# Optimization experiments

Measured on AMD Instinct MI355X. Metric: run time of the kernel, lower is better.

Reference implementation:

```python
import jax, jax.numpy as jnp
import numpy as np

# EntNet entity-memory update (Henaff et al. 2017), per selected entity i:
#   g_i      = sigmoid(s . h_i + s . w_i)                       (gate)
#   h~_i     = relu(h_i @ U^T + w_i @ V^T + s @ W^T)            (candidate)
#   h_i      = l2_normalize(h_i + g_i * h~_i)
# The original TF code loops over `indices` in Python; since each index touches a
# distinct entity slot, the updates are independent and we vectorize with a single
# gather over the entity axis and a scatter (.at[].set) back.

def setup_inputs() -> dict:
    key = jax.random.key(0)
    ks = jax.random.split(key, 6)
    B, N, D, K = 32, 1024, 1024, 512
    return {
        "encoded_sents": jax.random.normal(ks[0], (B, D), jnp.float32),
        "hiddens": jax.random.normal(ks[1], (B, N, D), jnp.float32),
        "keys": jax.random.normal(ks[2], (B, N, D), jnp.float32),
        "U": jax.random.normal(ks[3], (D, D), jnp.float32),
        "V": jax.random.normal(ks[4], (D, D), jnp.float32),
        "W": jax.random.normal(ks[5], (D, D), jnp.float32),
        "indices": jnp.arange(K, dtype=jnp.int64),
    }

def reference(encoded_sents, hiddens, keys, U, V, W, indices):
    EPS = 1e-12
    h = hiddens[:, indices, :]                     # [B,K,D] gather selected entities
    w = keys[:, indices, :]                        # [B,K,D]
    s = encoded_sents                              # [B,D]
    # gate: sigmoid(s.h_i + s.w_i) -> [B,K]
    g = jax.nn.sigmoid(jnp.einsum('bd,bkd->bk', s, h + w))
    # candidate: relu(h U^T + w V^T + s W^T) -> [B,K,D]
    h_tilde = jax.nn.relu(
        jnp.einsum('bkd,ed->bke', h, U)
        + jnp.einsum('bkd,ed->bke', w, V)
        + (s @ W.T)[:, None, :]
    )
    h_new = h + g[..., None] * h_tilde
    # tf.math.l2_normalize: x * rsqrt(max(sum(x^2), eps))
    h_new = h_new * jax.lax.rsqrt(jnp.maximum(jnp.sum(h_new * h_new, axis=-1, keepdims=True), EPS))
    # scatter updated entities back
    return hiddens.at[:, indices, :].set(h_new)
```

## Files before the change

kernel.cpp:

```cpp
#include <hip/hip_runtime.h>

constexpr int Bb = 32;
constexpr int Nn = 1024;
constexpr int Dd = 1024;
constexpr int Kk = 512;
constexpr int Mm = Bb * Kk;
constexpr int KD = 2 * Dd;

using bf16x8 = __bf16 __attribute__((ext_vector_type(8)));
using f32x4  = float __attribute__((ext_vector_type(4)));

constexpr size_t WS_BBF = 0;
constexpr size_t WS_G   = (size_t)4 * 1024 * 1024;
constexpr size_t WS_SW  = WS_G + 64 * 1024;
constexpr size_t WS_RN  = WS_SW + 128 * 1024;

__global__ void prep_b_kernel(const float* __restrict__ U,
                              const float* __restrict__ V,
                              __bf16* __restrict__ Bbf) {
  int t = blockIdx.x * 256 + threadIdx.x;
  int e = t >> 8;
  int c = (t & 255) << 3;
  const float* src = (c < Dd) ? (U + (size_t)e * Dd + c)
                              : (V + (size_t)e * Dd + (c - Dd));
  f32x4 f0 = *(const f32x4*)src;
  f32x4 f1 = *(const f32x4*)(src + 4);
  bf16x8 v;
  v[0] = (__bf16)f0[0]; v[1] = (__bf16)f0[1]; v[2] = (__bf16)f0[2]; v[3] = (__bf16)f0[3];
  v[4] = (__bf16)f1[0]; v[5] = (__bf16)f1[1]; v[6] = (__bf16)f1[2]; v[7] = (__bf16)f1[3];
  *(bf16x8*)(Bbf + (size_t)e * KD + c) = v;
}

__global__ void sw_kernel(const float* __restrict__ s,
                          const float* __restrict__ W,
                          float* __restrict__ sW) {
  int e = blockIdx.x * 4 + (threadIdx.x >> 6);
  int lane = threadIdx.x & 63;
  const float* wp = W + (size_t)e * Dd;
  float wr[16];
#pragma unroll
  for (int c = 0; c < 4; c++) {
    f32x4 wv = *(const f32x4*)(wp + c * 256 + lane * 4);
    wr[c*4+0] = wv[0]; wr[c*4+1] = wv[1]; wr[c*4+2] = wv[2]; wr[c*4+3] = wv[3];
  }
  for (int b = 0; b < Bb; b++) {
    const float* sp = s + (size_t)b * Dd;
    float acc = 0.f;
#pragma unroll
    for (int c = 0; c < 4; c++) {
      f32x4 sv = *(const f32x4*)(sp + c * 256 + lane * 4);
      acc += sv[0]*wr[c*4+0] + sv[1]*wr[c*4+1] + sv[2]*wr[c*4+2] + sv[3]*wr[c*4+3];
    }
#pragma unroll
    for (int off = 32; off; off >>= 1) acc += __shfl_xor(acc, off);
    if (lane == 0) sW[b * Nn + e] = acc;
  }
}

__global__ void g_kernel(const float* __restrict__ s,
                         const float* __restrict__ hiddens,
                         const float* __restrict__ keys,
                         const int* __restrict__ idx,
                         float* __restrict__ g) {
  int wid = blockIdx.x * 4 + (threadIdx.x >> 6);
  int lane = threadIdx.x & 63;
  int b = wid >> 9;
  int k = wid & (Kk - 1);
  int row = idx[k];
  const float* hp = hiddens + ((size_t)(b * Nn + row)) * Dd;
  const float* wp = keys    + ((size_t)(b * Nn + row)) * Dd;
  const float* sp = s + (size_t)b * Dd;
  float acc = 0.f;
#pragma unroll
  for (int c = 0; c < 4; c++) {
    int d = c * 256 + lane * 4;
    f32x4 hv = *(const f32x4*)(hp + d);
    f32x4 wv = *(const f32x4*)(wp + d);
    f32x4 sv = *(const f32x4*)(sp + d);
    acc += sv[0]*(hv[0]+wv[0]) + sv[1]*(hv[1]+wv[1])
         + sv[2]*(hv[2]+wv[2]) + sv[3]*(hv[3]+wv[3]);
  }
#pragma unroll
  for (int off = 32; off; off >>= 1) acc += __shfl_xor(acc, off);
  if (lane == 0) g[wid] = 1.f / (1.f + expf(-acc));
}

__global__ __launch_bounds__(256)
void gemm_kernel(const float* __restrict__ hiddens,
                 const float* __restrict__ keys,
                 const int* __restrict__ idx,
                 const __bf16* __restrict__ Bbf,
                 const float* __restrict__ sW,
                 const float* __restrict__ g,
                 float* __restrict__ rownorm,
                 float* __restrict__ out) {
  __shared__ __bf16 a_lds[128 * 64];
  __shared__ __bf16 b_lds[128 * 64];

  int bid = blockIdx.x;
  int mt = bid >> 3;
  int nt = bid & 7;
  int m0 = mt * 128, e0 = nt * 128;
  int tid = threadIdx.x, lane = tid & 63, wave = tid >> 6;

  size_t roff[4]; int prow[4], pcol[4];
#pragma unroll
  for (int i = 0; i < 4; i++) {
    int p = tid + i * 256;
    int row = p >> 3;
    pcol[i] = (p & 7) * 8;
    prow[i] = row;
    int m = m0 + row;
    int b = m >> 9;
    int r = idx[m & (Kk - 1)];
    roff[i] = ((size_t)(b * Nn + r)) * Dd;
  }
  int bofs[4], brow[4], bcolb[4];
#pragma unroll
  for (int i = 0; i < 4; i++) {
    int o = (wave * 4 + i) * 1024 + lane * 16;
    bofs[i] = o;
    brow[i] = o >> 7;
    bcolb[i] = o & 127;
  }

  f32x4 acc[4][4] = {};
  int wm = (wave >> 1) * 64, we = (wave & 1) * 64;
  int lr = lane & 15, lg = lane >> 4;
  const char* BbfB = (const char*)Bbf;

  for (int t = 0; t < KD / 64; ++t) {
    int kd0 = t * 64;
    const float* Asrc = (kd0 < Dd) ? hiddens : keys;
    int d0 = kd0 & (Dd - 1);

#pragma unroll
    for (int i = 0; i < 4; i++) {
      const void* gp = BbfB + ((size_t)(e0 + brow[i]) * KD + kd0) * 2 + bcolb[i];
      __builtin_amdgcn_global_load_lds(
          (const __attribute__((address_space(1))) void*)gp,
          (__attribute__((address_space(3))) void*)((char*)b_lds + bofs[i]),
          16, 0, 0);
    }
#pragma unroll
    for (int i = 0; i < 4; i++) {
      const float* src = Asrc + roff[i] + d0 + pcol[i];
      f32x4 f0 = *(const f32x4*)src;
      f32x4 f1 = *(const f32x4*)(src + 4);
      bf16x8 v;
      v[0]=(__bf16)f0[0]; v[1]=(__bf16)f0[1]; v[2]=(__bf16)f0[2]; v[3]=(__bf16)f0[3];
      v[4]=(__bf16)f1[0]; v[5]=(__bf16)f1[1]; v[6]=(__bf16)f1[2]; v[7]=(__bf16)f1[3];
      *(bf16x8*)&a_lds[prow[i] * 64 + pcol[i]] = v;
    }
    __syncthreads();

#pragma unroll
    for (int kh = 0; kh < 2; ++kh) {
      bf16x8 af[4], bfr[4];
#pragma unroll
      for (int i = 0; i < 4; i++)
        af[i] = *(const bf16x8*)&a_lds[(wm + i * 16 + lr) * 64 + kh * 32 + lg * 8];
#pragma unroll
      for (int j = 0; j < 4; j++)
        bfr[j] = *(const bf16x8*)&b_lds[(we + j * 16 + lr) * 64 + kh * 32 + lg * 8];
#pragma unroll
      for (int i = 0; i < 4; i++)
#pragma unroll
        for (int j = 0; j < 4; j++)
          acc[i][j] = __builtin_amdgcn_mfma_f32_16x16x32_bf16(af[i], bfr[j], acc[i][j], 0, 0, 0);
    }
    __syncthreads();
  }

#pragma unroll
  for (int i = 0; i < 4; i++) {
#pragma unroll
    for (int r = 0; r < 4; r++) {
      int m = m0 + wm + i * 16 + lg * 4 + r;
      int b = m >> 9;
      int rowidx = idx[m & (Kk - 1)];
      size_t base = ((size_t)(b * Nn + rowidx)) * Dd;
      float gg = g[m];
      float part = 0.f;
#pragma unroll
      for (int j = 0; j < 4; j++) {
        int e = e0 + we + j * 16 + lr;
        float ht = acc[i][j][r] + sW[b * Nn + e];
        ht = fmaxf(ht, 0.f);
        float v = hiddens[base + e] + gg * ht;
        out[base + e] = v;
        part += v * v;
      }
      part += __shfl_xor(part, 1);
      part += __shfl_xor(part, 2);
      part += __shfl_xor(part, 4);
      part += __shfl_xor(part, 8);
      if (lr == 0) atomicAdd(&rownorm[m], part);
    }
  }
}

__global__ void norm_kernel(const int* __restrict__ idx,
                            const float* __restrict__ rownorm,
                            float* __restrict__ out) {
  int m = blockIdx.x;
  int b = m >> 9;
  int rowidx = idx[m & (Kk - 1)];
  float nr = fmaxf(rownorm[m], 1e-12f);
  float y = rsqrtf(nr);
  y = y * (1.5f - 0.5f * nr * y * y);
  f32x4* p = (f32x4*)(out + ((size_t)(b * Nn + rowidx)) * Dd);
  f32x4 v = p[threadIdx.x];
  v[0] *= y; v[1] *= y; v[2] *= y; v[3] *= y;
  p[threadIdx.x] = v;
}

extern "C" void kernel_launch(void* const* d_in, const int* in_sizes, int n_in,
                              void* d_out, int out_size, void* d_ws, size_t ws_size,
                              hipStream_t stream) {
  const float* s       = (const float*)d_in[0];
  const float* hiddens = (const float*)d_in[1];
  const float* keys    = (const float*)d_in[2];
  const float* U       = (const float*)d_in[3];
  const float* V       = (const float*)d_in[4];
  const float* W       = (const float*)d_in[5];
  const int*   idx     = (const int*)d_in[6];
  float* out = (float*)d_out;

  char* ws = (char*)d_ws;
  __bf16* Bbf    = (__bf16*)(ws + WS_BBF);
  float*  g      = (float*)(ws + WS_G);
  float*  sW     = (float*)(ws + WS_SW);
  float*  rnorm  = (float*)(ws + WS_RN);

  hipMemcpyAsync(out, hiddens, (size_t)out_size * sizeof(float),
                 hipMemcpyDeviceToDevice, stream);
  hipMemsetAsync(rnorm, 0, Mm * sizeof(float), stream);
  prep_b_kernel<<<1024, 256, 0, stream>>>(U, V, Bbf);
  sw_kernel<<<Nn / 4, 256, 0, stream>>>(s, W, sW);
  g_kernel<<<Mm / 4, 256, 0, stream>>>(s, hiddens, keys, idx, g);
  gemm_kernel<<<(Mm / 128) * (Nn / 128), 256, 0, stream>>>(
      hiddens, keys, idx, Bbf, sW, g, rnorm, out);
  norm_kernel<<<Mm, 256, 0, stream>>>(idx, rnorm, out);
}
```

Before: 540.4 us.

## Pre-pack gathered A to bf16, async-load both GEMM operands, copy only unselected rows

The gate kernel now also converts the gathered h and w rows to a contiguous bf16 A matrix. The GEMM then streams both operands straight into LDS with global_load_lds instead of converting fp32 in registers. The full hiddens memcpy is replaced by a masked copy kernel that skips rows the GEMM overwrites. The tile order is changed so consecutive blocks share the same B column tile. The cost is a 64MB bf16 workspace write and read, plus extra mask and copy kernel launches.

New measurement: 519.4 us. -3.9%, faster.

```diff
diff --git a/kernel.cpp b/kernel.cpp
--- a/kernel.cpp
+++ b/kernel.cpp
@@ -10,10 +10,29 @@
 using bf16x8 = __bf16 __attribute__((ext_vector_type(8)));
 using f32x4  = float __attribute__((ext_vector_type(4)));
 
-constexpr size_t WS_BBF = 0;
-constexpr size_t WS_G   = (size_t)4 * 1024 * 1024;
-constexpr size_t WS_SW  = WS_G + 64 * 1024;
-constexpr size_t WS_RN  = WS_SW + 128 * 1024;
+constexpr size_t WS_ABF  = 0;
+constexpr size_t WS_BBF  = (size_t)Mm * KD * 2;
+constexpr size_t WS_G    = WS_BBF + (size_t)Nn * KD * 2;
+constexpr size_t WS_SW   = WS_G + Mm * sizeof(float);
+constexpr size_t WS_RN   = WS_SW + Bb * Nn * sizeof(float);
+constexpr size_t WS_MASK = WS_RN + Mm * sizeof(float);
+
+__global__ void mask_kernel(const int* __restrict__ idx, int* __restrict__ mask) {
+  int t = threadIdx.x;
+  mask[t] = 0;
+  __syncthreads();
+  if (t < Kk) mask[idx[t]] = 1;
+}
+
+__global__ void copy_kernel(const float* __restrict__ hiddens,
+                            const int* __restrict__ mask,
+                            float* __restrict__ out) {
+  int bid = blockIdx.x;
+  int n = bid & (Nn - 1);
+  if (mask[n]) return;
+  size_t base = (size_t)bid * Dd + threadIdx.x * 4;
+  *(f32x4*)(out + base) = *(const f32x4*)(hiddens + base);
+}
 
 __global__ void prep_b_kernel(const float* __restrict__ U,
                               const float* __restrict__ V,
@@ -57,100 +76,96 @@
   }
 }
 
-__global__ void g_kernel(const float* __restrict__ s,
-                         const float* __restrict__ hiddens,
-                         const float* __restrict__ keys,
-                         const int* __restrict__ idx,
-                         float* __restrict__ g) {
-  int wid = blockIdx.x * 4 + (threadIdx.x >> 6);
+__global__ void pack_g_kernel(const float* __restrict__ s,
+                              const float* __restrict__ hiddens,
+                              const float* __restrict__ keys,
+                              const int* __restrict__ idx,
+                              __bf16* __restrict__ Abf,
+                              float* __restrict__ g) {
+  int m = blockIdx.x * 4 + (threadIdx.x >> 6);
   int lane = threadIdx.x & 63;
-  int b = wid >> 9;
-  int k = wid & (Kk - 1);
+  int b = m >> 9;
+  int k = m & (Kk - 1);
   int row = idx[k];
   const float* hp = hiddens + ((size_t)(b * Nn + row)) * Dd;
   const float* wp = keys    + ((size_t)(b * Nn + row)) * Dd;
   const float* sp = s + (size_t)b * Dd;
+  __bf16* ap = Abf + (size_t)m * KD;
+
   float acc = 0.f;
 #pragma unroll
-  for (int c = 0; c < 4; c++) {
-    int d = c * 256 + lane * 4;
-    f32x4 hv = *(const f32x4*)(hp + d);
-    f32x4 wv = *(const f32x4*)(wp + d);
-    f32x4 sv = *(const f32x4*)(sp + d);
-    acc += sv[0]*(hv[0]+wv[0]) + sv[1]*(hv[1]+wv[1])
-         + sv[2]*(hv[2]+wv[2]) + sv[3]*(hv[3]+wv[3]);
+  for (int c = 0; c < 2; c++) {
+    int d = c * 512 + lane * 8;
+    f32x4 h0 = *(const f32x4*)(hp + d);
+    f32x4 h1 = *(const f32x4*)(hp + d + 4);
+    f32x4 w0 = *(const f32x4*)(wp + d);
+    f32x4 w1 = *(const f32x4*)(wp + d + 4);
+    f32x4 s0 = *(const f32x4*)(sp + d);
+    f32x4 s1 = *(const f32x4*)(sp + d + 4);
+    acc += s0[0]*(h0[0]+w0[0]) + s0[1]*(h0[1]+w0[1])
+         + s0[2]*(h0[2]+w0[2]) + s0[3]*(h0[3]+w0[3])
+         + s1[0]*(h1[0]+w1[0]) + s1[1]*(h1[1]+w1[1])
+         + s1[2]*(h1[2]+w1[2]) + s1[3]*(h1[3]+w1[3]);
+    bf16x8 hv, wv;
+    hv[0]=(__bf16)h0[0]; hv[1]=(__bf16)h0[1]; hv[2]=(__bf16)h0[2]; hv[3]=(__bf16)h0[3];
+    hv[4]=(__bf16)h1[0]; hv[5]=(__bf16)h1[1]; hv[6]=(__bf16)h1[2]; hv[7]=(__bf16)h1[3];
+    wv[0]=(__bf16)w0[0]; wv[1]=(__bf16)w0[1]; wv[2]=(__bf16)w0[2]; wv[3]=(__bf16)w0[3];
+    wv[4]=(__bf16)w1[0]; wv[5]=(__bf16)w1[1]; wv[6]=(__bf16)w1[2]; wv[7]=(__bf16)w1[3];
+    *(bf16x8*)(ap + d) = hv;
+    *(bf16x8*)(ap + Dd + d) = wv;
   }
 #pragma unroll
   for (int off = 32; off; off >>= 1) acc += __shfl_xor(acc, off);
-  if (lane == 0) g[wid] = 1.f / (1.f + expf(-acc));
+  if (lane == 0) g[m] = 1.f / (1.f + expf(-acc));
 }
 
 __global__ __launch_bounds__(256)
-void gemm_kernel(const float* __restrict__ hiddens,
-                 const float* __restrict__ keys,
+void gemm_kernel(const __bf16* __restrict__ Abf,
+                 const __bf16* __restrict__ Bbf,
                  const int* __restrict__ idx,
-                 const __bf16* __restrict__ Bbf,
                  const float* __restrict__ sW,
                  const float* __restrict__ g,
+                 const float* __restrict__ hiddens,
                  float* __restrict__ rownorm,
                  float* __restrict__ out) {
   __shared__ __bf16 a_lds[128 * 64];
   __shared__ __bf16 b_lds[128 * 64];
 
   int bid = blockIdx.x;
-  int mt = bid >> 3;
-  int nt = bid & 7;
+  int mt = bid & 127;
+  int nt = bid >> 7;
   int m0 = mt * 128, e0 = nt * 128;
   int tid = threadIdx.x, lane = tid & 63, wave = tid >> 6;
 
-  size_t roff[4]; int prow[4], pcol[4];
-#pragma unroll
-  for (int i = 0; i < 4; i++) {
-    int p = tid + i * 256;
-    int row = p >> 3;
-    pcol[i] = (p & 7) * 8;
-    prow[i] = row;
-    int m = m0 + row;
-    int b = m >> 9;
-    int r = idx[m & (Kk - 1)];
-    roff[i] = ((size_t)(b * Nn + r)) * Dd;
-  }
-  int bofs[4], brow[4], bcolb[4];
+  int lofs[4]; size_t aoff[4], boff[4];
 #pragma unroll
   for (int i = 0; i < 4; i++) {
     int o = (wave * 4 + i) * 1024 + lane * 16;
-    bofs[i] = o;
-    brow[i] = o >> 7;
-    bcolb[i] = o & 127;
+    lofs[i] = o;
+    int row = o >> 7;
+    int colb = o & 127;
+    aoff[i] = ((size_t)(m0 + row) * KD) * 2 + colb;
+    boff[i] = ((size_t)(e0 + row) * KD) * 2 + colb;
   }
 
   f32x4 acc[4][4] = {};
   int wm = (wave >> 1) * 64, we = (wave & 1) * 64;
   int lr = lane & 15, lg = lane >> 4;
-  const char* BbfB = (const char*)Bbf;
+  const char* Ab = (const char*)Abf;
+  const char* Bbp = (const char*)Bbf;
 
   for (int t = 0; t < KD / 64; ++t) {
-    int kd0 = t * 64;
-    const float* Asrc = (kd0 < Dd) ? hiddens : keys;
-    int d0 = kd0 & (Dd - 1);
-
+    size_t kb = (size_t)t * 128;
 #pragma unroll
     for (int i = 0; i < 4; i++) {
-      const void* gp = BbfB + ((size_t)(e0 + brow[i]) * KD + kd0) * 2 + bcolb[i];
       __builtin_amdgcn_global_load_lds(
-          (const __attribute__((address_space(1))) void*)gp,
-          (__attribute__((address_space(3))) void*)((char*)b_lds + bofs[i]),
+          (const __attribute__((address_space(1))) void*)(Ab + aoff[i] + kb),
+          (__attribute__((address_space(3))) void*)((char*)a_lds + lofs[i]),
           16, 0, 0);
-    }
-#pragma unroll
-    for (int i = 0; i < 4; i++) {
-      const float* src = Asrc + roff[i] + d0 + pcol[i];
-      f32x4 f0 = *(const f32x4*)src;
-      f32x4 f1 = *(const f32x4*)(src + 4);
-      bf16x8 v;
-      v[0]=(__bf16)f0[0]; v[1]=(__bf16)f0[1]; v[2]=(__bf16)f0[2]; v[3]=(__bf16)f0[3];
-      v[4]=(__bf16)f1[0]; v[5]=(__bf16)f1[1]; v[6]=(__bf16)f1[2]; v[7]=(__bf16)f1[3];
-      *(bf16x8*)&a_lds[prow[i] * 64 + pcol[i]] = v;
+      __builtin_amdgcn_global_load_lds(
+          (const __attribute__((address_space(1))) void*)(Bbp + boff[i] + kb),
+          (__attribute__((address_space(3))) void*)((char*)b_lds + lofs[i]),
+          16, 0, 0);
     }
     __syncthreads();
 
@@ -228,18 +243,20 @@
   float* out = (float*)d_out;
 
   char* ws = (char*)d_ws;
-  __bf16* Bbf    = (__bf16*)(ws + WS_BBF);
-  float*  g      = (float*)(ws + WS_G);
-  float*  sW     = (float*)(ws + WS_SW);
-  float*  rnorm  = (float*)(ws + WS_RN);
-
-  hipMemcpyAsync(out, hiddens, (size_t)out_size * sizeof(float),
-                 hipMemcpyDeviceToDevice, stream);
+  __bf16* Abf   = (__bf16*)(ws + WS_ABF);
+  __bf16* Bbf   = (__bf16*)(ws + WS_BBF);
+  float*  g     = (float*)(ws + WS_G);
+  float*  sW    = (float*)(ws + WS_SW);
+  float*  rnorm = (float*)(ws + WS_RN);
+  int*    mask  = (int*)(ws + WS_MASK);
+
   hipMemsetAsync(rnorm, 0, Mm * sizeof(float), stream);
+  mask_kernel<<<1, Nn, 0, stream>>>(idx, mask);
+  copy_kernel<<<Bb * Nn, 256, 0, stream>>>(hiddens, mask, out);
   prep_b_kernel<<<1024, 256, 0, stream>>>(U, V, Bbf);
   sw_kernel<<<Nn / 4, 256, 0, stream>>>(s, W, sW);
-  g_kernel<<<Mm / 4, 256, 0, stream>>>(s, hiddens, keys, idx, g);
+  pack_g_kernel<<<Mm / 4, 256, 0, stream>>>(s, hiddens, keys, idx, Abf, g);
   gemm_kernel<<<(Mm / 128) * (Nn / 128), 256, 0, stream>>>(
-      hiddens, keys, idx, Bbf, sW, g, rnorm, out);
+      Abf, Bbf, idx, sW, g, hiddens, rnorm, out);
   norm_kernel<<<Mm, 256, 0, stream>>>(idx, rnorm, out);
 }
```
